# Optimization experiments

Hardware: AMD Instinct MI355X
Metric: run time of the kernel (lower is better)

## Reference

```python
import jax, jax.numpy as jnp
import numpy as np

B, T, C, H, L, V = 4, 1024, 1024, 16, 6, 32000
D = C // H
STD = 0.02


def setup_inputs() -> dict:
    key = jax.random.key(0)
    ks = jax.random.split(key, 12)
    return {
        "idx": jax.random.randint(ks[0], (B, T), 0, V),
        "tok_emb": jax.random.normal(ks[1], (V, C), jnp.float32) * STD,
        "pos_emb": jax.random.normal(ks[2], (T, C), jnp.float32) * STD,
        "qkv_w": jax.random.normal(ks[3], (L, C, 3 * C), jnp.float32) * STD,
        "attn_out_w": jax.random.normal(ks[4], (L, C, C), jnp.float32) * STD,
        "attn_out_b": jnp.zeros((L, C), jnp.float32),
        "fc1_w": jax.random.normal(ks[5], (L, C, 4 * C), jnp.float32) * STD,
        "fc1_b": jnp.zeros((L, 4 * C), jnp.float32),
        "fc2_w": jax.random.normal(ks[6], (L, 4 * C, C), jnp.float32) * STD,
        "fc2_b": jnp.zeros((L, C), jnp.float32),
        "ln1_w": jnp.ones((L, C), jnp.float32),
        "ln1_b": jnp.zeros((L, C), jnp.float32),
        "ln2_w": jnp.ones((L, C), jnp.float32),
        "ln2_b": jnp.zeros((L, C), jnp.float32),
        "lnf_w": jnp.ones((C,), jnp.float32),
        "lnf_b": jnp.zeros((C,), jnp.float32),
        "head_w": jax.random.normal(ks[7], (C, V), jnp.float32) * STD,
    }


def layernorm(x, w, b, eps=1e-5):
    mu = jnp.mean(x, axis=-1, keepdims=True)
    var = jnp.var(x, axis=-1, keepdims=True)
    return (x - mu) * jax.lax.rsqrt(var + eps) * w + b


def attention(x, qkv_w, out_w, out_b, causal_mask):
    # x: (B,T,C)
    qkv = jnp.einsum("btc,cf->btf", x, qkv_w)  # (B,T,3C)
    q, k, v = jnp.split(qkv, 3, axis=-1)
    q = q.reshape(B, T, H, D).transpose(0, 2, 1, 3)  # (B,H,T,D)
    k = k.reshape(B, T, H, D).transpose(0, 2, 1, 3)
    v = v.reshape(B, T, H, D).transpose(0, 2, 1, 3)
    scores = jnp.einsum("bhqd,bhkd->bhqk", q, k) / np.sqrt(D).astype(np.float32)
    scores = jnp.where(causal_mask, scores, -jnp.inf)
    w = jax.nn.softmax(scores, axis=-1)
    out = jnp.einsum("bhqk,bhkd->bhqd", w, v)  # (B,H,T,D)
    out = out.transpose(0, 2, 1, 3).reshape(B, T, C)
    return jnp.einsum("btc,cd->btd", out, out_w) + out_b


def reference(idx, tok_emb, pos_emb, qkv_w, attn_out_w, attn_out_b,
              fc1_w, fc1_b, fc2_w, fc2_b, ln1_w, ln1_b, ln2_w, ln2_b,
              lnf_w, lnf_b, head_w):
    causal_mask = jnp.tril(jnp.ones((T, T), dtype=bool))[None, None]  # (1,1,T,T)
    x = tok_emb[idx] + pos_emb[jnp.arange(T)][None]  # (B,T,C)
    for l in range(L):
        h = layernorm(x, ln1_w[l], ln1_b[l])
        x = x + attention(h, qkv_w[l], attn_out_w[l], attn_out_b[l], causal_mask)
        h = layernorm(x, ln2_w[l], ln2_b[l])
        h = jax.nn.relu(jnp.einsum("btc,cf->btf", h, fc1_w[l]) + fc1_b[l])
        x = x + jnp.einsum("btf,fc->btc", h, fc2_w[l]) + fc2_b[l]
    x = layernorm(x, lnf_w, lnf_b)
    logits = jnp.einsum("btc,cv->btv", x, head_w)  # (B,T,V)
    return logits
```

## Files before the change

kernel.cpp:

```cpp
#include <hip/hip_runtime.h>
#include <cstdint>
#include <cstddef>

typedef __bf16 bf16_t;
typedef __bf16 bf16x8 __attribute__((ext_vector_type(8)));
typedef float f32x4 __attribute__((ext_vector_type(4)));
typedef int i32x4 __attribute__((ext_vector_type(4)));

#define B_ 4
#define T_ 1024
#define C_ 1024
#define H_ 16
#define L_ 6
#define V_ 32000
#define M_ (B_ * T_)

__global__ __launch_bounds__(256) void k_embed(const int* __restrict__ idx,
                                               const float* __restrict__ tok,
                                               const float* __restrict__ pos,
                                               float* __restrict__ x) {
  int row = blockIdx.x;
  int t = row & (T_ - 1);
  int id = idx[row];
  int c = threadIdx.x * 4;
  f32x4 a = *(const f32x4*)(tok + (size_t)id * C_ + c);
  f32x4 p = *(const f32x4*)(pos + (size_t)t * C_ + c);
  *(f32x4*)(x + (size_t)row * C_ + c) = a + p;
}

__global__ __launch_bounds__(256) void k_ln(const float* __restrict__ x,
                                            const float* __restrict__ w,
                                            const float* __restrict__ b,
                                            bf16_t* __restrict__ out) {
  __shared__ float red[8];
  int row = blockIdx.x;
  int tid = threadIdx.x;
  const float* xr = x + (size_t)row * C_;
  f32x4 v = *(const f32x4*)(xr + tid * 4);
  float s = v[0] + v[1] + v[2] + v[3];
  float q = v[0] * v[0] + v[1] * v[1] + v[2] * v[2] + v[3] * v[3];
#pragma unroll
  for (int off = 32; off; off >>= 1) {
    s += __shfl_xor(s, off);
    q += __shfl_xor(q, off);
  }
  int wid = tid >> 6;
  if ((tid & 63) == 0) { red[wid * 2] = s; red[wid * 2 + 1] = q; }
  __syncthreads();
  s = red[0] + red[2] + red[4] + red[6];
  q = red[1] + red[3] + red[5] + red[7];
  float mu = s * (1.f / C_);
  float var = q * (1.f / C_) - mu * mu;
  float rstd = rsqrtf(var + 1e-5f);
  f32x4 wv = *(const f32x4*)(w + tid * 4);
  f32x4 bv = *(const f32x4*)(b + tid * 4);
  bf16_t* o = out + (size_t)row * C_ + tid * 4;
#pragma unroll
  for (int j = 0; j < 4; j++) o[j] = (bf16_t)((v[j] - mu) * rstd * wv[j] + bv[j]);
}

__global__ __launch_bounds__(256) void k_transpose_bf16(const float* __restrict__ in,
                                                        bf16_t* __restrict__ out,
                                                        int K, int N) {
  __shared__ float tile[32][33];
  int n0 = blockIdx.x * 32, k0 = blockIdx.y * 32;
  int tid = threadIdx.x;
  int cr = tid >> 5, cc = tid & 31;
#pragma unroll
  for (int it = 0; it < 4; it++) {
    int r = it * 8 + cr;
    tile[r][cc] = in[(size_t)(k0 + r) * N + n0 + cc];
  }
  __syncthreads();
#pragma unroll
  for (int it = 0; it < 4; it++) {
    int r = it * 8 + cr;
    out[(size_t)(n0 + r) * K + k0 + cc] = (bf16_t)tile[cc][r];
  }
}

__global__ __launch_bounds__(256) void k_transpose_layer(
    const float* __restrict__ qkvw, const float* __restrict__ attnw,
    const float* __restrict__ fc1w, const float* __restrict__ fc2w,
    bf16_t* __restrict__ qkvT, bf16_t* __restrict__ owT,
    bf16_t* __restrict__ fc1T, bf16_t* __restrict__ fc2T) {
  __shared__ float tile[32][33];
  int tb = blockIdx.x;
  const float* in;
  bf16_t* out;
  int K, N;
  bool qs = false;
  if (tb < 3072) { in = qkvw; out = qkvT; K = 1024; N = 3072; qs = true; }
  else if (tb < 4096) { tb -= 3072; in = attnw; out = owT; K = 1024; N = 1024; }
  else if (tb < 8192) { tb -= 4096; in = fc1w; out = fc1T; K = 1024; N = 4096; }
  else { tb -= 8192; in = fc2w; out = fc2T; K = 4096; N = 1024; }
  int nTx = N >> 5;
  int n0 = (tb % nTx) * 32, k0 = (tb / nTx) * 32;
  int tid = threadIdx.x;
  int cr = tid >> 5, cc = tid & 31;
#pragma unroll
  for (int it = 0; it < 4; it++) {
    int r = it * 8 + cr;
    tile[r][cc] = in[(size_t)(k0 + r) * N + n0 + cc];
  }
  __syncthreads();
#pragma unroll
  for (int it = 0; it < 4; it++) {
    int r = it * 8 + cr;
    float v = tile[cc][r];
    if (qs && (n0 + r) < 1024) v *= 0.125f;
    out[(size_t)(n0 + r) * K + k0 + cc] = (bf16_t)v;
  }
}

__global__ __launch_bounds__(256) void k_vtrans(const bf16_t* __restrict__ vh,
                                                bf16_t* __restrict__ vT) {
  __shared__ bf16_t tile[64][65];
  int bh = blockIdx.x;
  int t0 = blockIdx.y * 64;
  int tid = threadIdx.x;
  int c = tid & 63, rr = tid >> 6;
  const bf16_t* src = vh + ((size_t)bh * T_ + t0) * 64;
#pragma unroll
  for (int it = 0; it < 16; it++) {
    int r = it * 4 + rr;
    tile[r][c] = src[(size_t)r * 64 + c];
  }
  __syncthreads();
  bf16_t* dst = vT + (size_t)bh * 64 * T_ + t0;
#pragma unroll
  for (int it = 0; it < 16; it++) {
    int dr = it * 4 + rr;
    dst[(size_t)dr * T_ + c] = tile[c][dr];
  }
}

__global__ __launch_bounds__(256) void k_attn(const bf16_t* __restrict__ qh,
                                              const bf16_t* __restrict__ kh,
                                              const bf16_t* __restrict__ vT,
                                              bf16_t* __restrict__ outb) {
  __shared__ bf16_t p_lds[4][16 * 32];
  int tid = threadIdx.x, lane = tid & 63, wid = tid >> 6;
  int bh = blockIdx.x;
  int b = bh >> 4, h = bh & (H_ - 1);
  int qbase = blockIdx.y * 64 + wid * 16;
  const bf16_t* qp = qh + ((size_t)bh * T_ + qbase) * 64;
  const bf16_t* kp = kh + (size_t)bh * T_ * 64;
  const bf16_t* vp = vT + (size_t)bh * 64 * T_;
  int r = lane & 15, g = lane >> 4;

  bf16x8 qf0 = *(const bf16x8*)(qp + r * 64 + g * 8);
  bf16x8 qf1 = *(const bf16x8*)(qp + r * 64 + 32 + g * 8);

  f32x4 o[4];
  float m[4], l[4];
#pragma unroll
  for (int j = 0; j < 4; j++) { m[j] = -1e30f; l[j] = 0.f; o[j] = (f32x4){0.f, 0.f, 0.f, 0.f}; }

  int kv_end = qbase + 16;
  for (int jb = 0; jb < kv_end; jb += 32) {
    f32x4 s0 = (f32x4){0.f, 0.f, 0.f, 0.f};
    f32x4 s1 = (f32x4){0.f, 0.f, 0.f, 0.f};
    const bf16_t* kb0 = kp + (size_t)(jb + r) * 64 + g * 8;
    const bf16_t* kb1 = kb0 + 16 * 64;
    s0 = __builtin_amdgcn_mfma_f32_16x16x32_bf16(qf0, *(const bf16x8*)(kb0), s0, 0, 0, 0);
    s0 = __builtin_amdgcn_mfma_f32_16x16x32_bf16(qf1, *(const bf16x8*)(kb0 + 32), s0, 0, 0, 0);
    s1 = __builtin_amdgcn_mfma_f32_16x16x32_bf16(qf0, *(const bf16x8*)(kb1), s1, 0, 0, 0);
    s1 = __builtin_amdgcn_mfma_f32_16x16x32_bf16(qf1, *(const bf16x8*)(kb1 + 32), s1, 0, 0, 0);

    float p0[4], p1[4], fac[4];
#pragma unroll
    for (int j = 0; j < 4; j++) {
      int rowg = qbase + g * 4 + j;
      float v0 = s0[j], v1 = s1[j];
      if (jb + r > rowg) v0 = -1e30f;
      if (jb + 16 + r > rowg) v1 = -1e30f;
      float t = fmaxf(v0, v1);
      t = fmaxf(t, __shfl_xor(t, 1));
      t = fmaxf(t, __shfl_xor(t, 2));
      t = fmaxf(t, __shfl_xor(t, 4));
      t = fmaxf(t, __shfl_xor(t, 8));
      float nm = fmaxf(m[j], t);
      p0[j] = __expf(v0 - nm);
      p1[j] = __expf(v1 - nm);
      float f = __expf(m[j] - nm);
      float ts = p0[j] + p1[j];
      ts += __shfl_xor(ts, 1);
      ts += __shfl_xor(ts, 2);
      ts += __shfl_xor(ts, 4);
      ts += __shfl_xor(ts, 8);
      l[j] = l[j] * f + ts;
      m[j] = nm;
      fac[j] = f;
    }
    f32x4 fv = (f32x4){fac[0], fac[1], fac[2], fac[3]};
#pragma unroll
    for (int d = 0; d < 4; d++) o[d] *= fv;

    bf16_t* pl = p_lds[wid];
#pragma unroll
    for (int j = 0; j < 4; j++) {
      pl[(g * 4 + j) * 32 + r] = (bf16_t)p0[j];
      pl[(g * 4 + j) * 32 + 16 + r] = (bf16_t)p1[j];
    }
    bf16x8 pa = *(const bf16x8*)(pl + r * 32 + g * 8);
#pragma unroll
    for (int d = 0; d < 4; d++) {
      const bf16_t* vf = vp + (size_t)(d * 16 + r) * T_ + jb + g * 8;
      o[d] = __builtin_amdgcn_mfma_f32_16x16x32_bf16(pa, *(const bf16x8*)(vf), o[d], 0, 0, 0);
    }
  }

#pragma unroll
  for (int d = 0; d < 4; d++) {
#pragma unroll
    for (int j = 0; j < 4; j++) {
      float val = o[d][j] / l[j];
      outb[((size_t)(b * T_ + qbase + g * 4 + j)) * C_ + h * 64 + d * 16 + r] = (bf16_t)val;
    }
  }
}

__device__ __forceinline__ void gld_lds16(const bf16_t* g, bf16_t* l) {
  __builtin_amdgcn_global_load_lds((const __attribute__((address_space(1))) void*)g,
                                   (__attribute__((address_space(3))) void*)l, 16, 0, 0);
}
__device__ __forceinline__ bf16x8 lds_rd128(uint32_t addr) {
  i32x4 d;
  asm volatile("ds_read_b128 %0, %1" : "=v"(d) : "v"(addr));
  return __builtin_bit_cast(bf16x8, d);
}
#define BAR_() __builtin_amdgcn_s_barrier()
#define SCHED0_() __builtin_amdgcn_sched_barrier(0)
#define WLGN_(n)                                                           \
  do {                                                                     \
    asm volatile("s_waitcnt lgkmcnt(" #n ")" ::: "memory");                \
    SCHED0_();                                                             \
  } while (0)

template <int MODE, int HASB, int HASRELU, int HASRES>
__global__ __launch_bounds__(256, 2) void k_gemm(const bf16_t* __restrict__ A,
                                                 const bf16_t* __restrict__ Bt,
                                                 const float* __restrict__ bias,
                                                 const float* resid,
                                                 void* Cout, int M, int N, int K) {
  __shared__ bf16_t As[2][128][64];
  __shared__ bf16_t Bs[2][128][64];
  bf16_t* AsF = &As[0][0][0];
  bf16_t* BsF = &Bs[0][0][0];
  const uint32_t asb = (uint32_t)(uintptr_t)AsF;
  const uint32_t bsb = (uint32_t)(uintptr_t)BsF;

  int tid = threadIdx.x, lane = tid & 63, w = tid >> 6;
  int wr = w >> 1, wc = w & 1;
  int r15 = lane & 15, g4 = lane >> 4;

  int nwg = (int)(gridDim.x * gridDim.y);
  int bid = (int)(blockIdx.y * gridDim.x + blockIdx.x);
  int xcd = bid & 7, loc = bid >> 3;
  int q8 = nwg >> 3, r8 = nwg & 7;
  int swz = (xcd < r8) ? xcd * (q8 + 1) + loc : r8 * (q8 + 1) + (xcd - r8) * q8 + loc;
  int nY = M >> 7;
  int by = swz % nY, bx = swz / nY;
  size_t rowBase = (size_t)by * 128;
  size_t colBase = (size_t)bx * 128;

  int srowL = (lane >> 3);
  int scol = ((lane & 7) ^ srowL) * 8;

  uint32_t xm = (uint32_t)((r15 & 7) << 4);
  uint32_t offK0 = ((uint32_t)(g4 * 16)) ^ xm;
  uint32_t offK1 = ((uint32_t)(g4 * 16 + 64)) ^ xm;
  uint32_t aRd = asb + (uint32_t)((wr * 64 + r15) * 128);
  uint32_t bRd = bsb + (uint32_t)((wc * 64 + r15) * 128);

  f32x4 acc[4][4];
#pragma unroll
  for (int i = 0; i < 4; i++)
#pragma unroll
    for (int j = 0; j < 4; j++) acc[i][j] = (f32x4){0.f, 0.f, 0.f, 0.f};

  bf16x8 a0[4], a1[4], b0[4], b1[4];

#define KSTAGE_(tk, bufv)                                                            \
  do {                                                                               \
    _Pragma("unroll") for (int _q = 0; _q < 4; _q++) {                               \
      int _row = _q * 32 + w * 8 + srowL;                                            \
      const bf16_t* _ga = A + (rowBase + _row) * (size_t)K + (size_t)(tk)*64 + scol; \
      const bf16_t* _gb = Bt + (colBase + _row) * (size_t)K + (size_t)(tk)*64 + scol;\
      gld_lds16(_ga, AsF + (bufv)*8192 + _q * 2048 + w * 512);                       \
      gld_lds16(_gb, BsF + (bufv)*8192 + _q * 2048 + w * 512);                       \
    }                                                                                \
  } while (0)

#define KRDS_(aset, bset, kk, bufv)                                                  \
  do {                                                                               \
    uint32_t _off = (kk) ? offK1 : offK0;                                            \
    uint32_t _ab = aRd + (uint32_t)(bufv)*16384u + _off;                             \
    uint32_t _bb = bRd + (uint32_t)(bufv)*16384u + _off;                             \
    _Pragma("unroll") for (int _m = 0; _m < 4; _m++)                                 \
        aset[_m] = lds_rd128(_ab + _m * 2048);                                       \
    _Pragma("unroll") for (int _n = 0; _n < 4; _n++)                                 \
        bset[_n] = lds_rd128(_bb + _n * 2048);                                       \
  } while (0)

#define KMFH_(aset, bset)                                                            \
  do {                                                                               \
    __builtin_amdgcn_s_setprio(1);                                                   \
    _Pragma("unroll") for (int _m = 0; _m < 4; _m++)                                 \
        _Pragma("unroll") for (int _n = 0; _n < 4; _n++)                             \
            acc[_m][_n] = __builtin_amdgcn_mfma_f32_16x16x32_bf16(                   \
                aset[_m], bset[_n], acc[_m][_n], 0, 0, 0);                           \
    __builtin_amdgcn_s_setprio(0);                                                   \
  } while (0)

  KSTAGE_(0, 0);
  asm volatile("s_waitcnt vmcnt(0)" ::: "memory");
  BAR_();

  int NT = K >> 6;
  for (int kt = 0; kt < NT; ++kt) {
    int buf = kt & 1;
    bool pf = (kt + 1 < NT);
    if (pf) KSTAGE_(kt + 1, buf ^ 1);
    KRDS_(a0, b0, 0, buf);
    KRDS_(a1, b1, 1, buf);
    WLGN_(8);
    KMFH_(a0, b0);
    WLGN_(0);
    KMFH_(a1, b1);
    asm volatile("s_waitcnt vmcnt(0)" ::: "memory");
    BAR_();
  }

#pragma unroll
  for (int i = 0; i < 4; i++) {
    size_t row0 = rowBase + wr * 64 + i * 16 + g4 * 4;
#pragma unroll
    for (int j = 0; j < 4; j++) {
      size_t col = colBase + wc * 64 + j * 16 + r15;
      float bi = HASB ? bias[col] : 0.f;
#pragma unroll
      for (int q = 0; q < 4; q++) {
        size_t row = row0 + q;
        float v = acc[i][j][q] + bi;
        if (HASRELU) v = fmaxf(v, 0.f);
        if (HASRES) v += resid[row * (size_t)N + col];
        if (MODE == 2) {
          int part = (int)(col >> 10);
          int within = (int)col & 1023;
          int hh = within >> 6, dd = within & 63;
          int bb = (int)(row >> 10), tt = (int)row & 1023;
          bf16_t* dstp = (bf16_t*)Cout + (size_t)part * ((size_t)M_ * C_);
          dstp[(((size_t)(bb * 16 + hh)) * 1024 + tt) * 64 + dd] = (bf16_t)v;
        } else if (MODE == 1) {
          ((bf16_t*)Cout)[row * (size_t)N + col] = (bf16_t)v;
        } else {
          ((float*)Cout)[row * (size_t)N + col] = v;
        }
      }
    }
  }
#undef KSTAGE_
#undef KRDS_
#undef KMFH_
}

#define STAGE_(q, tk, bufv)                                                           \
  do {                                                                                \
    const bf16_t* _ga = A + (size_t)(rowBase + (q)*64 + srow) * (size_t)K +           \
                        (size_t)(tk)*64 + scol;                                       \
    const bf16_t* _gb = Bt + (size_t)(colBase + (q)*64 + srow) * (size_t)K +          \
                        (size_t)(tk)*64 + scol;                                       \
    gld_lds16(_ga, AsF + (bufv)*16384 + (q)*4096 + w * 512);                          \
    gld_lds16(_gb, BsF + (bufv)*16384 + (q)*4096 + w * 512);                          \
  } while (0)

#define RDS_(aset, bset, kk, bufv)                                                    \
  do {                                                                                \
    uint32_t _off = (kk) ? offK1 : offK0;                                             \
    uint32_t _ab = aRd + (uint32_t)(bufv)*32768u + _off;                              \
    uint32_t _bb = bRd + (uint32_t)(bufv)*32768u + _off;                              \
    _Pragma("unroll") for (int _m = 0; _m < 8; _m++)                                  \
        aset[_m] = lds_rd128(_ab + _m * 2048);                                        \
    _Pragma("unroll") for (int _n = 0; _n < 4; _n++)                                  \
        bset[_n] = lds_rd128(_bb + _n * 2048);                                        \
  } while (0)

#define MFH_(aset, bset)                                                              \
  do {                                                                                \
    __builtin_amdgcn_s_setprio(1);                                                    \
    _Pragma("unroll") for (int _m = 0; _m < 8; _m++)                                  \
        _Pragma("unroll") for (int _n = 0; _n < 4; _n++)                              \
            acc[_m][_n] = __builtin_amdgcn_mfma_f32_16x16x32_bf16(                    \
                aset[_m], bset[_n], acc[_m][_n], 0, 0, 0);                            \
    __builtin_amdgcn_s_setprio(0);                                                    \
  } while (0)

template <int OUTBF, int HASB, int HASRELU, int HASRES>
__global__ __launch_bounds__(512, 2) void k_gemm256(const bf16_t* __restrict__ A,
                                                    const bf16_t* __restrict__ Bt,
                                                    const float* __restrict__ bias,
                                                    const float* resid,
                                                    void* Cout, int M, int N, int K) {
  __shared__ bf16_t As[2][256][64];
  __shared__ bf16_t Bs[2][256][64];
  bf16_t* AsF = &As[0][0][0];
  bf16_t* BsF = &Bs[0][0][0];
  const uint32_t asb = (uint32_t)(uintptr_t)AsF;
  const uint32_t bsb = (uint32_t)(uintptr_t)BsF;

  int tid = threadIdx.x, lane = tid & 63, w = tid >> 6;
  int wr = w >> 2, wc = w & 3;
  int r15 = lane & 15, g4 = lane >> 4;

  int nwg = (int)gridDim.x;
  int bid = (int)blockIdx.x;
  int xcd = bid & 7, loc = bid >> 3;
  int q8 = nwg >> 3, r8 = nwg & 7;
  int swz = (xcd < r8) ? xcd * (q8 + 1) + loc : r8 * (q8 + 1) + (xcd - r8) * q8 + loc;
  int nY = M >> 8;
  int by = swz % nY, bx = swz / nY;
  int rowBase = by * 256, colBase = bx * 256;

  int srow = w * 8 + (lane >> 3);
  int scol = ((lane & 7) ^ (lane >> 3)) * 8;

  uint32_t xm = (uint32_t)((r15 & 7) << 4);
  uint32_t offK0 = ((uint32_t)(g4 * 16)) ^ xm;
  uint32_t offK1 = ((uint32_t)(g4 * 16 + 64)) ^ xm;
  uint32_t aRd = asb + (uint32_t)((wr * 128 + r15) * 128);
  uint32_t bRd = bsb + (uint32_t)((wc * 64 + r15) * 128);

  f32x4 acc[8][4];
#pragma unroll
  for (int i = 0; i < 8; i++)
#pragma unroll
    for (int j = 0; j < 4; j++) acc[i][j] = (f32x4){0.f, 0.f, 0.f, 0.f};

  bf16x8 a0[8], a1[8], b0[4], b1[4];

#pragma unroll
  for (int q = 0; q < 4; q++) STAGE_(q, 0, 0);
  asm volatile("s_waitcnt vmcnt(0)" ::: "memory");
  BAR_();

  int NT = K >> 6;
  for (int kt = 0; kt < NT; ++kt) {
    int buf = kt & 1;
    bool pf = (kt + 1 < NT);
    if (pf) {
#pragma unroll
      for (int q = 0; q < 4; q++) STAGE_(q, kt + 1, buf ^ 1);
    }
    RDS_(a0, b0, 0, buf);
    RDS_(a1, b1, 1, buf);
    WLGN_(12);
    MFH_(a0, b0);
    WLGN_(0);
    MFH_(a1, b1);
    asm volatile("s_waitcnt vmcnt(0)" ::: "memory");
    BAR_();
  }

#pragma unroll
  for (int m = 0; m < 8; m++) {
    size_t row0 = (size_t)rowBase + wr * 128 + m * 16 + g4 * 4;
#pragma unroll
    for (int n = 0; n < 4; n++) {
      size_t col = (size_t)colBase + wc * 64 + n * 16 + r15;
      float bi = HASB ? bias[col] : 0.f;
#pragma unroll
      for (int qq = 0; qq < 4; qq++) {
        size_t row = row0 + qq;
        float v = acc[m][n][qq] + bi;
        if (HASRELU) v = fmaxf(v, 0.f);
        if (HASRES) v += resid[row * (size_t)N + col];
        if (OUTBF)
          ((bf16_t*)Cout)[row * (size_t)N + col] = (bf16_t)v;
        else
          ((float*)Cout)[row * (size_t)N + col] = v;
      }
    }
  }
}

extern "C" void kernel_launch(void* const* d_in, const int* in_sizes, int n_in,
                              void* d_out, int out_size, void* d_ws, size_t ws_size,
                              hipStream_t stream) {
  (void)in_sizes; (void)n_in; (void)out_size; (void)ws_size;
  const int* idx = (const int*)d_in[0];
  const float* tok_emb = (const float*)d_in[1];
  const float* pos_emb = (const float*)d_in[2];
  const float* qkv_w = (const float*)d_in[3];
  const float* attn_out_w = (const float*)d_in[4];
  const float* attn_out_b = (const float*)d_in[5];
  const float* fc1_w = (const float*)d_in[6];
  const float* fc1_b = (const float*)d_in[7];
  const float* fc2_w = (const float*)d_in[8];
  const float* fc2_b = (const float*)d_in[9];
  const float* ln1_w = (const float*)d_in[10];
  const float* ln1_b = (const float*)d_in[11];
  const float* ln2_w = (const float*)d_in[12];
  const float* ln2_b = (const float*)d_in[13];
  const float* lnf_w = (const float*)d_in[14];
  const float* lnf_b = (const float*)d_in[15];
  const float* head_w = (const float*)d_in[16];
  float* out = (float*)d_out;

  char* wsp = (char*)d_ws;
  auto alloc = [&](size_t bytes) {
    char* p = wsp;
    wsp += (bytes + 255) & ~(size_t)255;
    return p;
  };
  float* x      = (float*)alloc((size_t)M_ * C_ * 4);
  bf16_t* hbuf  = (bf16_t*)alloc((size_t)M_ * C_ * 2);
  bf16_t* qhb   = (bf16_t*)alloc((size_t)3 * M_ * C_ * 2);
  bf16_t* khb   = qhb + (size_t)M_ * C_;
  bf16_t* vhb   = khb + (size_t)M_ * C_;
  bf16_t* vTb   = (bf16_t*)alloc((size_t)M_ * C_ * 2);
  bf16_t* attnb = (bf16_t*)alloc((size_t)M_ * C_ * 2);
  bf16_t* midb  = (bf16_t*)alloc((size_t)M_ * 4 * C_ * 2);
  bf16_t* qkvwT = (bf16_t*)alloc((size_t)3 * C_ * C_ * 2);
  bf16_t* owT   = (bf16_t*)alloc((size_t)C_ * C_ * 2);
  bf16_t* fc1wT = (bf16_t*)alloc((size_t)4 * C_ * C_ * 2);
  bf16_t* fc2wT = (bf16_t*)alloc((size_t)4 * C_ * C_ * 2);
  bf16_t* headwT= (bf16_t*)alloc((size_t)C_ * V_ * 2);

  k_embed<<<M_, 256, 0, stream>>>(idx, tok_emb, pos_emb, x);
  k_transpose_bf16<<<dim3(V_ / 32, C_ / 32), 256, 0, stream>>>(head_w, headwT, C_, V_);

  for (int l = 0; l < L_; l++) {
    k_transpose_layer<<<12288, 256, 0, stream>>>(
        qkv_w + (size_t)l * C_ * 3 * C_, attn_out_w + (size_t)l * C_ * C_,
        fc1_w + (size_t)l * C_ * 4 * C_, fc2_w + (size_t)l * 4 * C_ * C_,
        qkvwT, owT, fc1wT, fc2wT);

    k_ln<<<M_, 256, 0, stream>>>(x, ln1_w + l * C_, ln1_b + l * C_, hbuf);
    k_gemm<2, 0, 0, 0><<<dim3(3 * C_ / 128, M_ / 128), 256, 0, stream>>>(
        hbuf, qkvwT, nullptr, nullptr, qhb, M_, 3 * C_, C_);
    k_vtrans<<<dim3(B_ * H_, T_ / 64), 256, 0, stream>>>(vhb, vTb);
    k_attn<<<dim3(B_ * H_, T_ / 64), 256, 0, stream>>>(qhb, khb, vTb, attnb);
    k_gemm<0, 1, 0, 1><<<dim3(C_ / 128, M_ / 128), 256, 0, stream>>>(
        attnb, owT, attn_out_b + l * C_, x, x, M_, C_, C_);

    k_ln<<<M_, 256, 0, stream>>>(x, ln2_w + l * C_, ln2_b + l * C_, hbuf);
    k_gemm<1, 1, 1, 0><<<dim3(4 * C_ / 128, M_ / 128), 256, 0, stream>>>(
        hbuf, fc1wT, fc1_b + (size_t)l * 4 * C_, nullptr, midb, M_, 4 * C_, C_);
    k_gemm<0, 1, 0, 1><<<dim3(C_ / 128, M_ / 128), 256, 0, stream>>>(
        midb, fc2wT, fc2_b + l * C_, x, x, M_, C_, 4 * C_);
  }

  k_ln<<<M_, 256, 0, stream>>>(x, lnf_w, lnf_b, hbuf);
  k_gemm256<0, 0, 0, 0><<<dim3((V_ / 256) * (M_ / 256)), 512, 0, stream>>>(
      hbuf, headwT, nullptr, nullptr, out, M_, V_, C_);
}
```

Before: 2.056 ms.

## Fuse V transpose into QKV GEMM epilogue and widen attention KV tile

The QKV GEMM epilogue now writes V directly in transposed (head, dim, token) layout using packed 4-element stores, so the separate k_vtrans kernel and its buffer are removed. The attention loop processes 64 keys per iteration instead of 32, halving the online-softmax reductions per key and skipping causal masking on fully unmasked blocks. The P staging buffer is padded to a 72-element stride. Risks include more register pressure in attention and strided V stores in the GEMM epilogue.

```diff
diff --git a/kernel.cpp b/kernel.cpp
--- a/kernel.cpp
+++ b/kernel.cpp
@@ -6,6 +6,7 @@
 typedef __bf16 bf16x8 __attribute__((ext_vector_type(8)));
 typedef float f32x4 __attribute__((ext_vector_type(4)));
 typedef int i32x4 __attribute__((ext_vector_type(4)));
+typedef short short4v __attribute__((ext_vector_type(4)));
 
 #define B_ 4
 #define T_ 1024
@@ -113,33 +114,11 @@
   }
 }
 
-__global__ __launch_bounds__(256) void k_vtrans(const bf16_t* __restrict__ vh,
-                                                bf16_t* __restrict__ vT) {
-  __shared__ bf16_t tile[64][65];
-  int bh = blockIdx.x;
-  int t0 = blockIdx.y * 64;
-  int tid = threadIdx.x;
-  int c = tid & 63, rr = tid >> 6;
-  const bf16_t* src = vh + ((size_t)bh * T_ + t0) * 64;
-#pragma unroll
-  for (int it = 0; it < 16; it++) {
-    int r = it * 4 + rr;
-    tile[r][c] = src[(size_t)r * 64 + c];
-  }
-  __syncthreads();
-  bf16_t* dst = vT + (size_t)bh * 64 * T_ + t0;
-#pragma unroll
-  for (int it = 0; it < 16; it++) {
-    int dr = it * 4 + rr;
-    dst[(size_t)dr * T_ + c] = tile[c][dr];
-  }
-}
-
 __global__ __launch_bounds__(256) void k_attn(const bf16_t* __restrict__ qh,
                                               const bf16_t* __restrict__ kh,
                                               const bf16_t* __restrict__ vT,
                                               bf16_t* __restrict__ outb) {
-  __shared__ bf16_t p_lds[4][16 * 32];
+  __shared__ bf16_t p_lds[4][16 * 72];
   int tid = threadIdx.x, lane = tid & 63, wid = tid >> 6;
   int bh = blockIdx.x;
   int b = bh >> 4, h = bh & (H_ - 1);
@@ -158,33 +137,42 @@
   for (int j = 0; j < 4; j++) { m[j] = -1e30f; l[j] = 0.f; o[j] = (f32x4){0.f, 0.f, 0.f, 0.f}; }
 
   int kv_end = qbase + 16;
-  for (int jb = 0; jb < kv_end; jb += 32) {
-    f32x4 s0 = (f32x4){0.f, 0.f, 0.f, 0.f};
-    f32x4 s1 = (f32x4){0.f, 0.f, 0.f, 0.f};
-    const bf16_t* kb0 = kp + (size_t)(jb + r) * 64 + g * 8;
-    const bf16_t* kb1 = kb0 + 16 * 64;
-    s0 = __builtin_amdgcn_mfma_f32_16x16x32_bf16(qf0, *(const bf16x8*)(kb0), s0, 0, 0, 0);
-    s0 = __builtin_amdgcn_mfma_f32_16x16x32_bf16(qf1, *(const bf16x8*)(kb0 + 32), s0, 0, 0, 0);
-    s1 = __builtin_amdgcn_mfma_f32_16x16x32_bf16(qf0, *(const bf16x8*)(kb1), s1, 0, 0, 0);
-    s1 = __builtin_amdgcn_mfma_f32_16x16x32_bf16(qf1, *(const bf16x8*)(kb1 + 32), s1, 0, 0, 0);
-
-    float p0[4], p1[4], fac[4];
+  for (int jb = 0; jb < kv_end; jb += 64) {
+    f32x4 s[4];
+#pragma unroll
+    for (int t = 0; t < 4; t++) s[t] = (f32x4){0.f, 0.f, 0.f, 0.f};
+    const bf16_t* kb = kp + (size_t)(jb + r) * 64 + g * 8;
+#pragma unroll
+    for (int t = 0; t < 4; t++) {
+      const bf16_t* kt = kb + (size_t)t * 16 * 64;
+      s[t] = __builtin_amdgcn_mfma_f32_16x16x32_bf16(qf0, *(const bf16x8*)(kt), s[t], 0, 0, 0);
+      s[t] = __builtin_amdgcn_mfma_f32_16x16x32_bf16(qf1, *(const bf16x8*)(kt + 32), s[t], 0, 0, 0);
+    }
+
+    bool needMask = (jb + 63 > qbase);
+    float pv[4][4], fac[4];
 #pragma unroll
     for (int j = 0; j < 4; j++) {
       int rowg = qbase + g * 4 + j;
-      float v0 = s0[j], v1 = s1[j];
-      if (jb + r > rowg) v0 = -1e30f;
-      if (jb + 16 + r > rowg) v1 = -1e30f;
-      float t = fmaxf(v0, v1);
-      t = fmaxf(t, __shfl_xor(t, 1));
-      t = fmaxf(t, __shfl_xor(t, 2));
-      t = fmaxf(t, __shfl_xor(t, 4));
-      t = fmaxf(t, __shfl_xor(t, 8));
-      float nm = fmaxf(m[j], t);
-      p0[j] = __expf(v0 - nm);
-      p1[j] = __expf(v1 - nm);
+      float v0 = s[0][j], v1 = s[1][j], v2 = s[2][j], v3 = s[3][j];
+      if (needMask) {
+        if (jb + r > rowg) v0 = -1e30f;
+        if (jb + 16 + r > rowg) v1 = -1e30f;
+        if (jb + 32 + r > rowg) v2 = -1e30f;
+        if (jb + 48 + r > rowg) v3 = -1e30f;
+      }
+      float t0 = fmaxf(fmaxf(v0, v1), fmaxf(v2, v3));
+      t0 = fmaxf(t0, __shfl_xor(t0, 1));
+      t0 = fmaxf(t0, __shfl_xor(t0, 2));
+      t0 = fmaxf(t0, __shfl_xor(t0, 4));
+      t0 = fmaxf(t0, __shfl_xor(t0, 8));
+      float nm = fmaxf(m[j], t0);
+      pv[j][0] = __expf(v0 - nm);
+      pv[j][1] = __expf(v1 - nm);
+      pv[j][2] = __expf(v2 - nm);
+      pv[j][3] = __expf(v3 - nm);
       float f = __expf(m[j] - nm);
-      float ts = p0[j] + p1[j];
+      float ts = (pv[j][0] + pv[j][1]) + (pv[j][2] + pv[j][3]);
       ts += __shfl_xor(ts, 1);
       ts += __shfl_xor(ts, 2);
       ts += __shfl_xor(ts, 4);
@@ -199,15 +187,18 @@
 
     bf16_t* pl = p_lds[wid];
 #pragma unroll
-    for (int j = 0; j < 4; j++) {
-      pl[(g * 4 + j) * 32 + r] = (bf16_t)p0[j];
-      pl[(g * 4 + j) * 32 + 16 + r] = (bf16_t)p1[j];
-    }
-    bf16x8 pa = *(const bf16x8*)(pl + r * 32 + g * 8);
+    for (int j = 0; j < 4; j++)
+#pragma unroll
+      for (int t = 0; t < 4; t++)
+        pl[(g * 4 + j) * 72 + t * 16 + r] = (bf16_t)pv[j][t];
+
+    bf16x8 pa0 = *(const bf16x8*)(pl + r * 72 + g * 8);
+    bf16x8 pa1 = *(const bf16x8*)(pl + r * 72 + 32 + g * 8);
 #pragma unroll
     for (int d = 0; d < 4; d++) {
       const bf16_t* vf = vp + (size_t)(d * 16 + r) * T_ + jb + g * 8;
-      o[d] = __builtin_amdgcn_mfma_f32_16x16x32_bf16(pa, *(const bf16x8*)(vf), o[d], 0, 0, 0);
+      o[d] = __builtin_amdgcn_mfma_f32_16x16x32_bf16(pa0, *(const bf16x8*)(vf), o[d], 0, 0, 0);
+      o[d] = __builtin_amdgcn_mfma_f32_16x16x32_bf16(pa1, *(const bf16x8*)(vf + 32), o[d], 0, 0, 0);
     }
   }
 
@@ -340,23 +331,41 @@
     for (int j = 0; j < 4; j++) {
       size_t col = colBase + wc * 64 + j * 16 + r15;
       float bi = HASB ? bias[col] : 0.f;
-#pragma unroll
-      for (int q = 0; q < 4; q++) {
-        size_t row = row0 + q;
-        float v = acc[i][j][q] + bi;
-        if (HASRELU) v = fmaxf(v, 0.f);
-        if (HASRES) v += resid[row * (size_t)N + col];
-        if (MODE == 2) {
-          int part = (int)(col >> 10);
-          int within = (int)col & 1023;
-          int hh = within >> 6, dd = within & 63;
-          int bb = (int)(row >> 10), tt = (int)row & 1023;
+      if (MODE == 2) {
+        float vv[4];
+#pragma unroll
+        for (int q = 0; q < 4; q++) vv[q] = acc[i][j][q];
+        int part = (int)(col >> 10);
+        int within = (int)col & 1023;
+        int hh = within >> 6, dd = within & 63;
+        int bb = (int)(row0 >> 10), tt = (int)row0 & 1023;
+        size_t bhh = (size_t)(bb * 16 + hh);
+        if (part < 2) {
           bf16_t* dstp = (bf16_t*)Cout + (size_t)part * ((size_t)M_ * C_);
-          dstp[(((size_t)(bb * 16 + hh)) * 1024 + tt) * 64 + dd] = (bf16_t)v;
-        } else if (MODE == 1) {
-          ((bf16_t*)Cout)[row * (size_t)N + col] = (bf16_t)v;
+#pragma unroll
+          for (int q = 0; q < 4; q++)
+            dstp[(bhh * 1024 + tt + q) * 64 + dd] = (bf16_t)vv[q];
         } else {
-          ((float*)Cout)[row * (size_t)N + col] = v;
+          bf16_t* dstp = (bf16_t*)Cout + 2 * ((size_t)M_ * C_);
+          short4v pk;
+#pragma unroll
+          for (int q = 0; q < 4; q++) {
+            bf16_t bv = (bf16_t)vv[q];
+            pk[q] = __builtin_bit_cast(short, bv);
+          }
+          *(short4v*)(dstp + (bhh * 64 + dd) * 1024 + tt) = pk;
+        }
+      } else {
+#pragma unroll
+        for (int q = 0; q < 4; q++) {
+          size_t row = row0 + q;
+          float v = acc[i][j][q] + bi;
+          if (HASRELU) v = fmaxf(v, 0.f);
+          if (HASRES) v += resid[row * (size_t)N + col];
+          if (MODE == 1)
+            ((bf16_t*)Cout)[row * (size_t)N + col] = (bf16_t)v;
+          else
+            ((float*)Cout)[row * (size_t)N + col] = v;
         }
       }
     }
@@ -518,8 +527,7 @@
   bf16_t* hbuf  = (bf16_t*)alloc((size_t)M_ * C_ * 2);
   bf16_t* qhb   = (bf16_t*)alloc((size_t)3 * M_ * C_ * 2);
   bf16_t* khb   = qhb + (size_t)M_ * C_;
-  bf16_t* vhb   = khb + (size_t)M_ * C_;
-  bf16_t* vTb   = (bf16_t*)alloc((size_t)M_ * C_ * 2);
+  bf16_t* vTb   = khb + (size_t)M_ * C_;
   bf16_t* attnb = (bf16_t*)alloc((size_t)M_ * C_ * 2);
   bf16_t* midb  = (bf16_t*)alloc((size_t)M_ * 4 * C_ * 2);
   bf16_t* qkvwT = (bf16_t*)alloc((size_t)3 * C_ * C_ * 2);
@@ -540,7 +548,6 @@
     k_ln<<<M_, 256, 0, stream>>>(x, ln1_w + l * C_, ln1_b + l * C_, hbuf);
     k_gemm<2, 0, 0, 0><<<dim3(3 * C_ / 128, M_ / 128), 256, 0, stream>>>(
         hbuf, qkvwT, nullptr, nullptr, qhb, M_, 3 * C_, C_);
-    k_vtrans<<<dim3(B_ * H_, T_ / 64), 256, 0, stream>>>(vhb, vTb);
     k_attn<<<dim3(B_ * H_, T_ / 64), 256, 0, stream>>>(qhb, khb, vTb, attnb);
     k_gemm<0, 1, 0, 1><<<dim3(C_ / 128, M_ / 128), 256, 0, stream>>>(
         attnb, owT, attn_out_b + l * C_, x, x, M_, C_, C_);
```

New measurement: 2.063 ms. About the same (+0.3%).
